# Performance work log

Measured on AMD Instinct MI355X. Metric: run time of the kernel, lower is better.

Reference implementation:

```python
import jax, jax.numpy as jnp
import numpy as np
import math

N, M = 50000, 32
ATOM_F = 128
NBR_F = 64
SH_DIM = 9  # (lmax+1)^2 with lmax=2


def setup_inputs() -> dict:
    key = jax.random.key(0)
    k = jax.random.split(key, 8)
    atom_fea = jax.random.normal(k[0], (N, ATOM_F), dtype=jnp.float32)
    nbr_fea = jax.random.normal(k[1], (N, M, NBR_F), dtype=jnp.float32)
    nbr_idx = jax.random.randint(k[2], (N, M), 0, N, dtype=jnp.int64)
    # radial MLP: Linear(NBR_F,NBR_F) -> Softplus -> Linear(NBR_F,SH_DIM)
    w1 = jax.random.normal(k[3], (NBR_F, NBR_F), dtype=jnp.float32) / np.sqrt(NBR_F)
    b1 = jnp.zeros((NBR_F,), dtype=jnp.float32)
    w2 = jax.random.normal(k[4], (NBR_F, SH_DIM), dtype=jnp.float32) / np.sqrt(NBR_F)
    b2 = jnp.zeros((SH_DIM,), dtype=jnp.float32)
    # FullyConnectedTensorProduct(ATOM_Fx0e, 0e+1o+2e, ATOM_Fx0e): the only
    # allowed path is 0e x 0e -> 0e, weight shape [ATOM_F, 1, ATOM_F] -> [ATOM_F, ATOM_F]
    tp_w = jax.random.normal(k[5], (ATOM_F, ATOM_F), dtype=jnp.float32)
    return {"atom_fea": atom_fea, "nbr_fea": nbr_fea, "nbr_idx": nbr_idx,
            "w1": w1, "b1": b1, "w2": w2, "b2": b2, "tp_w": tp_w}


def reference(atom_fea, nbr_fea, nbr_idx, w1, b1, w2, b2, tp_w):
    n, m, _ = nbr_fea.shape
    f = atom_fea.shape[1]
    idx = nbr_idx.reshape(-1)                      # [N*M]
    neigh = atom_fea[idx]                          # [N*M, F] gather
    radial = nbr_fea.reshape(n * m, -1)            # [N*M, NBR_F]
    R = jax.nn.softplus(radial @ w1 + b1) @ w2 + b2  # [N*M, SH_DIM]
    # pos=None path: Y = ones, so W = Y * R = R; only the 0e channel W[:,0]
    # couples in the tensor product. Path normalization: 1/sqrt(mul_in1*mul_in2).
    scalar = R[:, 0]                               # [N*M]
    msg = (neigh @ tp_w) * scalar[:, None] / math.sqrt(f)  # [N*M, F]
    # scatter-mean over neighbor indices (as in source: idx_i = nbr_idx.view(-1))
    sums = jax.ops.segment_sum(msg, idx, num_segments=n)   # [N, F]
    cnt = jax.ops.segment_sum(jnp.ones((n * m,), msg.dtype), idx, num_segments=n)
    out = sums / jnp.maximum(cnt, 1.0)[:, None]
    return out * 1.0  # scale = 1.0 ** 0.5
```

## Files before the change

kernel.cpp:

```cpp
#include <hip/hip_runtime.h>
#include <hip/hip_bf16.h>

#define NATOM 50000
#define MNBR  32
#define NEDGE (NATOM * MNBR)
#define ATOMF 128
#define NBRF  64
#define SHDIM 9

typedef float  f32x4  __attribute__((ext_vector_type(4)));
typedef __bf16 bf16x8 __attribute__((ext_vector_type(8)));

__device__ __forceinline__ float softplus_f(float x) {
    float e = __builtin_amdgcn_exp2f(-fabsf(x) * 1.44269504089f);
    float l = __builtin_amdgcn_logf(1.0f + e);
    return fmaxf(x, 0.0f) + 0.69314718056f * l;
}

__device__ __forceinline__ bf16x8 to_bf16x8(float4 lo, float4 hi) {
    bf16x8 r;
    r[0] = (__bf16)lo.x; r[1] = (__bf16)lo.y; r[2] = (__bf16)lo.z; r[3] = (__bf16)lo.w;
    r[4] = (__bf16)hi.x; r[5] = (__bf16)hi.y; r[6] = (__bf16)hi.z; r[7] = (__bf16)hi.w;
    return r;
}

__global__ __launch_bounds__(256, 4) void edge_kernel(
    const float* __restrict__ nbr_fea, const int* __restrict__ nbr_idx,
    const float* __restrict__ w1, const float* __restrict__ b1,
    const float* __restrict__ w2, const float* __restrict__ b2,
    float* __restrict__ S, float* __restrict__ C)
{
    const int lane = threadIdx.x & 63;
    const int m    = lane & 15;
    const int quad = lane >> 4;
    const int wave_id = (int)((blockIdx.x * blockDim.x + threadIdx.x) >> 6);
    const int nwaves  = (int)((gridDim.x * blockDim.x) >> 6);

    bf16x8 bfrag[2][4];
#pragma unroll
    for (int c = 0; c < 2; ++c)
#pragma unroll
        for (int nb = 0; nb < 4; ++nb)
#pragma unroll
            for (int j = 0; j < 8; ++j)
                bfrag[c][nb][j] = (__bf16)w1[(c * 32 + quad * 8 + j) * NBRF + nb * 16 + m];

    float b1v[4], w2v[4];
#pragma unroll
    for (int nb = 0; nb < 4; ++nb) {
        b1v[nb] = b1[nb * 16 + m];
        w2v[nb] = w2[(nb * 16 + m) * SHDIM + 0];
    }
    const float b2_0 = b2[0];

    const int ntiles = NEDGE / 16;
    for (int t = wave_id; t < ntiles; t += nwaves) {
        const int e0 = t * 16;

        bf16x8 afrag[2];
#pragma unroll
        for (int c = 0; c < 2; ++c) {
            const float* base = &nbr_fea[(size_t)(e0 + m) * NBRF + c * 32 + quad * 8];
            const float4 f0 = *(const float4*)(base);
            const float4 f1 = *(const float4*)(base + 4);
            afrag[c] = to_bf16x8(f0, f1);
        }

        f32x4 acc[4] = { {0.f,0.f,0.f,0.f}, {0.f,0.f,0.f,0.f},
                         {0.f,0.f,0.f,0.f}, {0.f,0.f,0.f,0.f} };
#pragma unroll
        for (int c = 0; c < 2; ++c)
#pragma unroll
            for (int nb = 0; nb < 4; ++nb)
                acc[nb] = __builtin_amdgcn_mfma_f32_16x16x32_bf16(
                    afrag[c], bfrag[c][nb], acc[nb], 0, 0, 0);

        float part[4] = {0.f, 0.f, 0.f, 0.f};
#pragma unroll
        for (int nb = 0; nb < 4; ++nb)
#pragma unroll
            for (int r = 0; r < 4; ++r)
                part[r] += softplus_f(acc[nb][r] + b1v[nb]) * w2v[nb];

#pragma unroll
        for (int off = 1; off < 16; off <<= 1)
#pragma unroll
            for (int r = 0; r < 4; ++r)
                part[r] += __shfl_xor(part[r], off, 64);

        if (m == 0) {
#pragma unroll
            for (int r = 0; r < 4; ++r) {
                const int e = e0 + quad * 4 + r;
                int j = nbr_idx[e];
                j = (j < 0) ? 0 : (j >= NATOM ? NATOM - 1 : j);
                atomicAdd(&S[j], part[r] + b2_0);
                atomicAdd(&C[j], 1.0f);
            }
        }
    }
}

__global__ __launch_bounds__(256) void atom_kernel(
    const float* __restrict__ atom_fea, const float* __restrict__ tp_w,
    const float* __restrict__ S, const float* __restrict__ C,
    float* __restrict__ out)
{
    const int lane = threadIdx.x & 63;
    const int wave = threadIdx.x >> 6;
    const int m    = lane & 15;
    const int quad = lane >> 4;

    bf16x8 bfrag[4][2];
#pragma unroll
    for (int c = 0; c < 4; ++c)
#pragma unroll
        for (int nb = 0; nb < 2; ++nb)
#pragma unroll
            for (int j = 0; j < 8; ++j)
                bfrag[c][nb][j] =
                    (__bf16)tp_w[(c * 32 + quad * 8 + j) * ATOMF + (wave * 2 + nb) * 16 + m];

    const int ntiles = NATOM / 16;
    for (int t = blockIdx.x; t < ntiles; t += gridDim.x) {
        const int j0 = t * 16;

        bf16x8 afrag[4];
#pragma unroll
        for (int c = 0; c < 4; ++c) {
            const float* base = &atom_fea[(size_t)(j0 + m) * ATOMF + c * 32 + quad * 8];
            const float4 f0 = *(const float4*)(base);
            const float4 f1 = *(const float4*)(base + 4);
            afrag[c] = to_bf16x8(f0, f1);
        }

        f32x4 acc[2] = { {0.f,0.f,0.f,0.f}, {0.f,0.f,0.f,0.f} };
#pragma unroll
        for (int c = 0; c < 4; ++c)
#pragma unroll
            for (int nb = 0; nb < 2; ++nb)
                acc[nb] = __builtin_amdgcn_mfma_f32_16x16x32_bf16(
                    afrag[c], bfrag[c][nb], acc[nb], 0, 0, 0);

        float sc[4];
#pragma unroll
        for (int r = 0; r < 4; ++r) {
            const int j = j0 + quad * 4 + r;
            sc[r] = S[j] / fmaxf(C[j], 1.0f) * 0.08838834764831843f;
        }

#pragma unroll
        for (int nb = 0; nb < 2; ++nb)
#pragma unroll
            for (int r = 0; r < 4; ++r)
                out[(size_t)(j0 + quad * 4 + r) * ATOMF + (wave * 2 + nb) * 16 + m] =
                    acc[nb][r] * sc[r];
    }
}

extern "C" void kernel_launch(void* const* d_in, const int* in_sizes, int n_in,
                              void* d_out, int out_size, void* d_ws, size_t ws_size,
                              hipStream_t stream) {
    const float* atom_fea = (const float*)d_in[0];
    const float* nbr_fea  = (const float*)d_in[1];
    const int*   nbr_idx  = (const int*)d_in[2];
    const float* w1       = (const float*)d_in[3];
    const float* b1       = (const float*)d_in[4];
    const float* w2       = (const float*)d_in[5];
    const float* b2       = (const float*)d_in[6];
    const float* tp_w     = (const float*)d_in[7];
    float* out = (float*)d_out;

    float* S  = (float*)d_ws;
    float* Cc = S + NATOM;

    hipMemsetAsync(d_ws, 0, 2 * NATOM * sizeof(float), stream);

    edge_kernel<<<2048, 256, 0, stream>>>(nbr_fea, nbr_idx, w1, b1, w2, b2, S, Cc);
    atom_kernel<<<1024, 256, 0, stream>>>(atom_fea, tp_w, S, Cc, out);
}
```

Before: 632.2 us.

## Replicate scatter accumulators and interleave sum/count to cut atomic contention

Edge kernel now writes sum and count interleaved in a single array and spreads blocks across up to 8 replicated copies chosen by block index, so fewer atomics collide on the same address. Neighbor indices are loaded once per 16-edge tile by 16 lanes, and the 16 per-edge values are redistributed so each of those lanes issues one atomic pair, instead of 4 lanes each issuing 4 pairs. The b2 bias is folded into the atom kernel as count*b2. In exchange there is a larger memset, and the atom kernel has to reduce across the replicas, with one lane per row doing the reads.

```diff
diff --git a/kernel.cpp b/kernel.cpp
--- a/kernel.cpp
+++ b/kernel.cpp
@@ -7,6 +7,7 @@
 #define ATOMF 128
 #define NBRF  64
 #define SHDIM 9
+#define NREP_MAX 8
 
 typedef float  f32x4  __attribute__((ext_vector_type(4)));
 typedef __bf16 bf16x8 __attribute__((ext_vector_type(8)));
@@ -27,8 +28,8 @@
 __global__ __launch_bounds__(256, 4) void edge_kernel(
     const float* __restrict__ nbr_fea, const int* __restrict__ nbr_idx,
     const float* __restrict__ w1, const float* __restrict__ b1,
-    const float* __restrict__ w2, const float* __restrict__ b2,
-    float* __restrict__ S, float* __restrict__ C)
+    const float* __restrict__ w2,
+    float* __restrict__ SC, int rep_mask)
 {
     const int lane = threadIdx.x & 63;
     const int m    = lane & 15;
@@ -36,6 +37,8 @@
     const int wave_id = (int)((blockIdx.x * blockDim.x + threadIdx.x) >> 6);
     const int nwaves  = (int)((gridDim.x * blockDim.x) >> 6);
 
+    float* mySC = SC + (size_t)(blockIdx.x & (unsigned)rep_mask) * (2 * NATOM);
+
     bf16x8 bfrag[2][4];
 #pragma unroll
     for (int c = 0; c < 2; ++c)
@@ -51,11 +54,16 @@
         b1v[nb] = b1[nb * 16 + m];
         w2v[nb] = w2[(nb * 16 + m) * SHDIM + 0];
     }
-    const float b2_0 = b2[0];
 
     const int ntiles = NEDGE / 16;
     for (int t = wave_id; t < ntiles; t += nwaves) {
         const int e0 = t * 16;
+
+        int jj = 0;
+        if (lane < 16) {
+            jj = nbr_idx[e0 + lane];
+            jj = (jj < 0) ? 0 : (jj >= NATOM ? NATOM - 1 : jj);
+        }
 
         bf16x8 afrag[2];
 #pragma unroll
@@ -88,28 +96,31 @@
             for (int r = 0; r < 4; ++r)
                 part[r] += __shfl_xor(part[r], off, 64);
 
-        if (m == 0) {
-#pragma unroll
-            for (int r = 0; r < 4; ++r) {
-                const int e = e0 + quad * 4 + r;
-                int j = nbr_idx[e];
-                j = (j < 0) ? 0 : (j >= NATOM ? NATOM - 1 : j);
-                atomicAdd(&S[j], part[r] + b2_0);
-                atomicAdd(&C[j], 1.0f);
-            }
+        const int src = ((lane & 15) >> 2) << 4;
+        const float t0 = __shfl(part[0], src, 64);
+        const float t1 = __shfl(part[1], src, 64);
+        const float t2 = __shfl(part[2], src, 64);
+        const float t3 = __shfl(part[3], src, 64);
+        const int rr = lane & 3;
+        const float val = (rr == 0) ? t0 : (rr == 1) ? t1 : (rr == 2) ? t2 : t3;
+
+        if (lane < 16) {
+            atomicAdd(&mySC[2 * jj],     val);
+            atomicAdd(&mySC[2 * jj + 1], 1.0f);
         }
     }
 }
 
 __global__ __launch_bounds__(256) void atom_kernel(
     const float* __restrict__ atom_fea, const float* __restrict__ tp_w,
-    const float* __restrict__ S, const float* __restrict__ C,
-    float* __restrict__ out)
+    const float* __restrict__ SC, const float* __restrict__ b2,
+    float* __restrict__ out, int nrep)
 {
     const int lane = threadIdx.x & 63;
     const int wave = threadIdx.x >> 6;
     const int m    = lane & 15;
     const int quad = lane >> 4;
+    const float b2_0 = b2[0];
 
     bf16x8 bfrag[4][2];
 #pragma unroll
@@ -142,12 +153,22 @@
                 acc[nb] = __builtin_amdgcn_mfma_f32_16x16x32_bf16(
                     afrag[c], bfrag[c][nb], acc[nb], 0, 0, 0);
 
-        float sc[4];
-#pragma unroll
-        for (int r = 0; r < 4; ++r) {
-            const int j = j0 + quad * 4 + r;
-            sc[r] = S[j] / fmaxf(C[j], 1.0f) * 0.08838834764831843f;
-        }
+        float sc[4] = {0.f, 0.f, 0.f, 0.f};
+        if (m == 0) {
+#pragma unroll
+            for (int r = 0; r < 4; ++r) {
+                const int j = j0 + quad * 4 + r;
+                float s = 0.f, c = 0.f;
+                for (int p = 0; p < nrep; ++p) {
+                    s += SC[(size_t)p * (2 * NATOM) + 2 * j];
+                    c += SC[(size_t)p * (2 * NATOM) + 2 * j + 1];
+                }
+                sc[r] = (s + c * b2_0) / fmaxf(c, 1.0f) * 0.08838834764831843f;
+            }
+        }
+#pragma unroll
+        for (int r = 0; r < 4; ++r)
+            sc[r] = __shfl(sc[r], quad << 4, 64);
 
 #pragma unroll
         for (int nb = 0; nb < 2; ++nb)
@@ -171,11 +192,12 @@
     const float* tp_w     = (const float*)d_in[7];
     float* out = (float*)d_out;
 
-    float* S  = (float*)d_ws;
-    float* Cc = S + NATOM;
-
-    hipMemsetAsync(d_ws, 0, 2 * NATOM * sizeof(float), stream);
-
-    edge_kernel<<<2048, 256, 0, stream>>>(nbr_fea, nbr_idx, w1, b1, w2, b2, S, Cc);
-    atom_kernel<<<1024, 256, 0, stream>>>(atom_fea, tp_w, S, Cc, out);
-}
+    float* SC = (float*)d_ws;
+
+    int nrep = (ws_size >= (size_t)NREP_MAX * 2 * NATOM * sizeof(float)) ? NREP_MAX : 1;
+
+    hipMemsetAsync(d_ws, 0, (size_t)nrep * 2 * NATOM * sizeof(float), stream);
+
+    edge_kernel<<<2048, 256, 0, stream>>>(nbr_fea, nbr_idx, w1, b1, w2, SC, nrep - 1);
+    atom_kernel<<<1024, 256, 0, stream>>>(atom_fea, tp_w, SC, b2, out, nrep);
+}
```

New measurement: 640.9 us. About the same (+1.4%).
